# Kernel optimization log

Hardware: AMD Instinct MI355X
Metric: run time of the kernel (lower is better)

Reference implementation:

```python
import jax, jax.numpy as jnp
import numpy as np

MUL0, MUL1, SCALARS_OUT = 16, 16, 128
L0, L1 = MUL0, MUL1 * 3            # 16, 48
PATH_NUMEL = MUL0 * MUL1 * SCALARS_OUT  # 32768 per path, two paths
EPS = 1e-5
# e3nn normalization: irrep_normalization='component' -> alpha = dim(ir_out) = 1;
# path_normalization='element' -> divide by sum over paths to same output of mul1*mul2 = 256+256 = 512.
PATH_COEFF = 1.0 / np.sqrt(512.0)
CG_110 = 1.0 / np.sqrt(3.0)  # wigner_3j(1,1,0)[i,j] = delta_ij/sqrt(3) (unit Frobenius norm)


def layer_norm(x, g, b):
    mu = jnp.mean(x, axis=-1, keepdims=True)
    var = jnp.mean(jnp.square(x - mu), axis=-1, keepdims=True)
    return (x - mu) * jax.lax.rsqrt(var + EPS) * g + b


def ff_block(x, g, b, w1, w2, b2):
    # LayerNorm -> Linear(no bias) -> SiLU -> Linear(bias); residual=False in both uses
    h = jax.nn.silu(layer_norm(x, g, b) @ w1)
    return h @ w2 + b2


def setup_inputs() -> dict:
    key = jax.random.key(0)
    ks = jax.random.split(key, 8)
    N = 2048
    return {
        "x": jax.random.normal(ks[0], (N, L0 + L1), dtype=jnp.float32),
        "we_ln_g": jnp.ones((L0,), jnp.float32),
        "we_ln_b": jnp.zeros((L0,), jnp.float32),
        "we_w1": jax.random.normal(ks[1], (L0, 4 * L0), jnp.float32) / np.sqrt(L0),
        "we_w2": jax.random.normal(ks[2], (4 * L0, 2 * PATH_NUMEL), jnp.float32) / np.sqrt(4 * L0),
        "we_b2": jnp.zeros((2 * PATH_NUMEL,), jnp.float32),
        "om_ln_g": jnp.ones((SCALARS_OUT,), jnp.float32),
        "om_ln_b": jnp.zeros((SCALARS_OUT,), jnp.float32),
        "om_w1": jax.random.normal(ks[3], (SCALARS_OUT, 4 * SCALARS_OUT), jnp.float32) / np.sqrt(SCALARS_OUT),
        "om_w2": jax.random.normal(ks[4], (4 * SCALARS_OUT, 1), jnp.float32) / np.sqrt(4 * SCALARS_OUT),
        "om_b2": jnp.zeros((1,), jnp.float32),
    }


def reference(x, we_ln_g, we_ln_b, we_w1, we_w2, we_b2,
              om_ln_g, om_ln_b, om_w1, om_w2, om_b2):
    N = x.shape[0]
    feats = x[:, :L0]                       # [N, 16] scalars (0e)
    x1 = x[:, L0:].reshape(N, MUL1, 3)      # [N, 16, 3] vectors (1o)

    # per-sample tensor-product weights (shared_weights=False)
    w = ff_block(feats, we_ln_g, we_ln_b, we_w1, we_w2, we_b2)  # [N, 65536]
    w0 = w[:, :PATH_NUMEL].reshape(N, MUL0, MUL0, SCALARS_OUT)
    w1 = w[:, PATH_NUMEL:].reshape(N, MUL1, MUL1, SCALARS_OUT)

    # path 0: 0e x 0e -> 0e  (uvw)
    o0 = jnp.einsum('nu,nv,nuvw->nw', feats, feats, w0)
    # path 1: 1o x 1o -> 0e  (uvw, CG = delta_ij/sqrt(3))
    o1 = jnp.einsum('nui,nvi,nuvw->nw', x1, x1, w1) * CG_110
    tp_out = PATH_COEFF * (o0 + o1)          # [N, 128]

    return ff_block(tp_out, om_ln_g, om_ln_b, om_w1, om_w2, om_b2)  # [N, 1]
```

## Files before the change

### kernel.cpp

```cpp
#include <hip/hip_runtime.h>
#include <hip/hip_bf16.h>
#include <cstdint>

#define EPS 1e-5f
#define PATH_COEFF 0.04419417382415922f
#define CG110     0.5773502691896258f

typedef __bf16 v8bf __attribute__((ext_vector_type(8)));
typedef float  v4f  __attribute__((ext_vector_type(4)));
typedef _Float16 v4h __attribute__((ext_vector_type(4)));
typedef unsigned int v4u __attribute__((ext_vector_type(4)));
typedef unsigned int v2u __attribute__((ext_vector_type(2)));

static __device__ __forceinline__ unsigned short f2bf(float x){
    unsigned int u = __builtin_bit_cast(unsigned int, x);
    u += 0x7fffu + ((u >> 16) & 1u);
    return (unsigned short)(u >> 16);
}
static __device__ __forceinline__ unsigned short f2h(float x){
    return __builtin_bit_cast(unsigned short, (_Float16)x);
}

__global__ __launch_bounds__(256)
void k_pre(const float* __restrict__ w2, const float* __restrict__ b2,
           unsigned short* __restrict__ Vt2,
           const float* __restrict__ om_w1, unsigned short* __restrict__ w1t,
           const float* __restrict__ x, const float* __restrict__ lng,
           const float* __restrict__ lnb, const float* __restrict__ we_w1,
           unsigned short* __restrict__ Q2, float* __restrict__ Ht, int N)
{
    __shared__ __align__(16) unsigned short tile[32][128];
    int b = blockIdx.x;
    int t = threadIdx.x;

    if (b < 260){
        int k    = b >> 2;
        int slab = b & 3;
        const float* srcbase = (k < 64) ? (w2 + (size_t)k * 65536) : b2;
        for (int chunk = 0; chunk < 4; ++chunk){
            int pbase = slab*128 + chunk*32;
            #pragma unroll
            for (int i = 0; i < 4; ++i){
                int g = t + 256*i;
                int ploc = g >> 5, c4 = g & 31;
                const float4 v = *(const float4*)(srcbase + (size_t)(pbase + ploc)*128 + c4*4);
                unsigned int w0 = (unsigned)f2bf(v.x) | ((unsigned)f2bf(v.y) << 16);
                unsigned int w1 = (unsigned)f2bf(v.z) | ((unsigned)f2bf(v.w) << 16);
                *(uint2*)&tile[ploc][c4*4] = make_uint2(w0, w1);
            }
            __syncthreads();
            int w = t & 127, h = t >> 7;
            int ps = slab*4 + chunk;
            unsigned int words[8];
            #pragma unroll
            for (int g2 = 0; g2 < 8; ++g2)
                words[g2] = (unsigned)tile[h*16 + g2*2][w] | ((unsigned)tile[h*16 + g2*2 + 1][w] << 16);
            unsigned short* dq0 = Vt2 + (((size_t)(k*16 + ps)*4 + 2*h    )*128 + w)*8;
            unsigned short* dq1 = Vt2 + (((size_t)(k*16 + ps)*4 + 2*h + 1)*128 + w)*8;
            *(uint4*)dq0 = make_uint4(words[0], words[1], words[2], words[3]);
            *(uint4*)dq1 = make_uint4(words[4], words[5], words[6], words[7]);
            __syncthreads();
        }
    } else if (b < 264){
        int j0 = (b - 260) * 128;
        for (int chunk = 0; chunk < 4; ++chunk){
            #pragma unroll
            for (int i = 0; i < 4; ++i){
                int g = t + 256*i;
                int wloc = g >> 5, c4 = g & 31;
                int w = chunk*32 + wloc;
                const float4 v = *(const float4*)(om_w1 + (size_t)w*512 + j0 + c4*4);
                unsigned int a = (unsigned)f2bf(v.x) | ((unsigned)f2bf(v.y) << 16);
                unsigned int bb = (unsigned)f2bf(v.z) | ((unsigned)f2bf(v.w) << 16);
                *(uint2*)&tile[wloc][c4*4] = make_uint2(a, bb);
            }
            __syncthreads();
            int jl = t & 127, h = t >> 7;
            unsigned int words[8];
            #pragma unroll
            for (int g2 = 0; g2 < 8; ++g2)
                words[g2] = (unsigned)tile[h*16 + g2*2][jl] | ((unsigned)tile[h*16 + g2*2 + 1][jl] << 16);
            unsigned short* dst = w1t + (size_t)(j0 + jl)*128 + chunk*32 + h*16;
            *(uint4*)dst       = make_uint4(words[0], words[1], words[2], words[3]);
            *(uint4*)(dst + 8) = make_uint4(words[4], words[5], words[6], words[7]);
            __syncthreads();
        }
    } else {
        int wv = t >> 6, lane = t & 63;
        int row = (b - 264)*4 + wv;
        const float* xr = x + (size_t)row * 64;
        float f[16]; float mu = 0.f;
        #pragma unroll
        for (int u = 0; u < 16; ++u){ f[u] = xr[u]; mu += f[u]; }
        mu *= (1.f/16.f);
        float var = 0.f;
        #pragma unroll
        for (int u = 0; u < 16; ++u){ float d = f[u] - mu; var += d*d; }
        var *= (1.f/16.f);
        float inv = rsqrtf(var + EPS);
        float lnf[16];
        #pragma unroll
        for (int u = 0; u < 16; ++u) lnf[u] = (f[u]-mu)*inv*lng[u] + lnb[u];
        float h1 = 0.f;
        #pragma unroll
        for (int u = 0; u < 16; ++u) h1 += lnf[u] * we_w1[u*64 + lane];
        float h = h1 / (1.f + expf(-h1));
        Ht[(size_t)lane * N + row] = h;
        if (lane == 0) Ht[(size_t)64 * N + row] = 1.f;

        union { unsigned short qs[8]; uint4 v; } qu;
        #pragma unroll
        for (int j = 0; j < 8; ++j){
            int p = lane*8 + j;
            float q;
            if (p < 256){
                int u = p >> 4, v = p & 15;
                q = PATH_COEFF * f[u] * f[v];
            } else {
                int pp = p - 256;
                int u = pp >> 4, v = pp & 15;
                const float* ya = xr + 16 + u*3;
                const float* yb = xr + 16 + v*3;
                q = (PATH_COEFF * CG110) * (ya[0]*yb[0] + ya[1]*yb[1] + ya[2]*yb[2]);
            }
            qu.qs[j] = f2bf(q);
        }
        int rb = row >> 6, r64 = row & 63;
        int ps = lane >> 2, quad4 = lane & 3;
        *(uint4*)(Q2 + (((size_t)(rb*16 + ps)*4 + quad4)*64 + r64)*8) = qu.v;
    }
}

__global__ __launch_bounds__(128, 4)
void k_main(const unsigned short* __restrict__ Q2, const unsigned short* __restrict__ Vt2,
            const float* __restrict__ Ht, unsigned short* __restrict__ partial, int N)
{
    __shared__ __align__(16) unsigned short Es[2][16*66];
    int kb = blockIdx.x % 65;
    int mb = blockIdx.x / 65;

    int tid  = threadIdx.x;
    int lane = tid & 63, wv = tid >> 6;
    int quad = lane >> 4, l16 = lane & 15;
    int rowbase = mb * 64;
    int wbase = wv * 64;

    const unsigned short* aroot = Q2  + (size_t)mb*32768 + quad*512  + l16*8;
    const unsigned short* broot = Vt2 + (size_t)kb*65536 + quad*1024 + (wbase + l16)*8;

    v4f acc[4][4];
    #pragma unroll
    for (int m=0;m<4;++m)
      #pragma unroll
      for (int n=0;n<4;++n)
        #pragma unroll
        for (int r=0;r<4;++r) acc[m][n][r] = 0.f;

    #pragma unroll 4
    for (int ps = 0; ps < 16; ++ps){
        const unsigned short* ap = aroot + ps*2048;
        const unsigned short* bp = broot + ps*4096;
        v8bf a[4], bb[4];
        #pragma unroll
        for (int m=0;m<4;++m) a[m]  = *(const v8bf*)(ap + m*128);
        #pragma unroll
        for (int n=0;n<4;++n) bb[n] = *(const v8bf*)(bp + n*128);
        #pragma unroll
        for (int m=0;m<4;++m)
          #pragma unroll
          for (int n=0;n<4;++n)
            acc[m][n] = __builtin_amdgcn_mfma_f32_16x16x32_bf16(a[m], bb[n], acc[m][n], 0, 0, 0);
    }

    const float* hp = Ht + (size_t)kb*N + rowbase + quad*4;
    unsigned short* my = Es[wv];
    unsigned short* gp = partial + (size_t)kb*N*128 + (size_t)rowbase*128 + wbase;
    #pragma unroll
    for (int m = 0; m < 4; ++m){
        v4f hv = *(const v4f*)(hp + m*16);
        #pragma unroll
        for (int n = 0; n < 4; ++n)
          #pragma unroll
          for (int r = 0; r < 4; ++r)
            my[(quad*4 + r)*66 + n*16 + l16] = f2h(hv[r]*acc[m][n][r]);
        #pragma unroll
        for (int jj = 0; jj < 2; ++jj){
            int idx = lane*2 + jj;
            int rr = idx >> 3, cc = idx & 7;
            v4u v = *(const v4u*)(Es[wv] + rr*66 + cc*8);
            __builtin_nontemporal_store(v, (v4u*)(gp + (size_t)(m*16 + rr)*128 + cc*8));
        }
    }
}

__global__ __launch_bounds__(128)
void k_red(const unsigned short* __restrict__ partial, const float* __restrict__ g,
           const float* __restrict__ b, unsigned short* __restrict__ lnf, int N)
{
    int t = threadIdx.x;
    int row0 = blockIdx.x * 4;
    int rl = t >> 5, w = (t & 31)*4;
    int row = row0 + rl;

    const unsigned short* p0 = partial + (size_t)row*128 + w;
    float s0=0.f, s1=0.f, s2=0.f, s3=0.f;
    #pragma unroll
    for (int sl = 0; sl < 65; ++sl){
        union { v2u u; v4h h; } cv;
        cv.u = __builtin_nontemporal_load((const v2u*)(p0 + (size_t)sl*N*128));
        s0 += (float)cv.h[0]; s1 += (float)cv.h[1]; s2 += (float)cv.h[2]; s3 += (float)cv.h[3];
    }
    float sum = s0+s1+s2+s3;
    float sq  = s0*s0+s1*s1+s2*s2+s3*s3;
    #pragma unroll
    for (int off=16; off>0; off>>=1){
        sum += __shfl_xor(sum, off, 32);
        sq  += __shfl_xor(sq,  off, 32);
    }
    float mu  = sum * (1.f/128.f);
    float var = sq * (1.f/128.f) - mu*mu;
    float inv = rsqrtf(var + EPS);
    unsigned short o[4];
    o[0] = f2bf((s0-mu)*inv*g[w+0] + b[w+0]);
    o[1] = f2bf((s1-mu)*inv*g[w+1] + b[w+1]);
    o[2] = f2bf((s2-mu)*inv*g[w+2] + b[w+2]);
    o[3] = f2bf((s3-mu)*inv*g[w+3] + b[w+3]);
    *(uint2*)(lnf + (size_t)row*128 + w) = *(uint2*)o;
}

__global__ __launch_bounds__(256)
void k_mlp2(const unsigned short* __restrict__ lnf, const unsigned short* __restrict__ w1t,
            const float* __restrict__ w2, const float* __restrict__ b2,
            float* __restrict__ out, int N)
{
    __shared__ float red2[4][64];
    int tid = threadIdx.x, lane = tid & 63, wv = tid >> 6;
    int quad = lane >> 4, l16 = lane & 15;
    int rowbase = blockIdx.x * 64;
    int jbase = wv * 128;

    v4f acc[4][8];
    #pragma unroll
    for (int m=0;m<4;++m)
      #pragma unroll
      for (int n=0;n<8;++n)
        #pragma unroll
        for (int r=0;r<4;++r) acc[m][n][r] = 0.f;

    #pragma unroll
    for (int ps = 0; ps < 4; ++ps){
        v8bf a[4], bb[8];
        #pragma unroll
        for (int m=0;m<4;++m)
            a[m]  = *(const v8bf*)(lnf + (size_t)(rowbase + m*16 + l16)*128 + ps*32 + quad*8);
        #pragma unroll
        for (int n=0;n<8;++n)
            bb[n] = *(const v8bf*)(w1t + (size_t)(jbase + n*16 + l16)*128 + ps*32 + quad*8);
        #pragma unroll
        for (int m=0;m<4;++m)
          #pragma unroll
          for (int n=0;n<8;++n)
            acc[m][n] = __builtin_amdgcn_mfma_f32_16x16x32_bf16(a[m], bb[n], acc[m][n], 0, 0, 0);
    }

    float w2v[8];
    #pragma unroll
    for (int n=0;n<8;++n) w2v[n] = w2[jbase + n*16 + l16];

    #pragma unroll
    for (int m=0;m<4;++m){
        #pragma unroll
        for (int r=0;r<4;++r){
            float s = 0.f;
            #pragma unroll
            for (int n=0;n<8;++n){
                float v = acc[m][n][r];
                s += (v / (1.f + expf(-v))) * w2v[n];
            }
            #pragma unroll
            for (int off=8; off>0; off>>=1) s += __shfl_xor(s, off, 16);
            if (l16 == 0) red2[wv][m*16 + quad*4 + r] = s;
        }
    }
    __syncthreads();
    if (tid < 64)
        out[rowbase + tid] = red2[0][tid] + red2[1][tid] + red2[2][tid] + red2[3][tid] + b2[0];
}

extern "C" void kernel_launch(void* const* d_in, const int* in_sizes, int n_in,
                              void* d_out, int out_size, void* d_ws, size_t ws_size,
                              hipStream_t stream)
{
    const float* x     = (const float*)d_in[0];
    const float* we_g  = (const float*)d_in[1];
    const float* we_b  = (const float*)d_in[2];
    const float* we_w1 = (const float*)d_in[3];
    const float* we_w2 = (const float*)d_in[4];
    const float* we_b2 = (const float*)d_in[5];
    const float* om_g  = (const float*)d_in[6];
    const float* om_b  = (const float*)d_in[7];
    const float* om_w1 = (const float*)d_in[8];
    const float* om_w2 = (const float*)d_in[9];
    const float* om_b2 = (const float*)d_in[10];

    int N  = in_sizes[0] / 64;

    char* ws = (char*)d_ws;
    size_t offV = 0;
    size_t szV  = (size_t)65*16*4*128*8*2;
    size_t offQ = offV + szV;
    size_t szQ  = (size_t)N*512*2;
    size_t offH = offQ + szQ;
    size_t szH  = (size_t)65*N*4;
    size_t offP = offH + szH;
    size_t szP  = (size_t)65*N*128*2;
    size_t offL = offP + szP;
    size_t szL  = (size_t)N*128*2;
    size_t offW = offL + szL;

    unsigned short* Vt2 = (unsigned short*)(ws + offV);
    unsigned short* Q2  = (unsigned short*)(ws + offQ);
    float* Ht           = (float*)(ws + offH);
    unsigned short* Par = (unsigned short*)(ws + offP);
    unsigned short* Lnf = (unsigned short*)(ws + offL);
    unsigned short* W1t = (unsigned short*)(ws + offW);
    float* out = (float*)d_out;

    hipLaunchKernelGGL(k_pre,  dim3(264 + N/4), dim3(256), 0, stream,
                       we_w2, we_b2, Vt2, om_w1, W1t, x, we_g, we_b, we_w1, Q2, Ht, N);
    hipLaunchKernelGGL(k_main, dim3(32*65),     dim3(128), 0, stream, Q2, Vt2, Ht, Par, N);
    hipLaunchKernelGGL(k_red,  dim3(N/4),       dim3(128), 0, stream, Par, om_g, om_b, Lnf, N);
    hipLaunchKernelGGL(k_mlp2, dim3(N/64),      dim3(256), 0, stream, Lnf, W1t, om_w2, om_b2, out, N);
}
```

Baseline: 151.9 us.

## Double-buffer B tiles through LDS and use 256-thread 2x2 wave blocks in k_main

Each k_main block now runs four waves arranged 2x2 over rows and columns, and the grid is halved to match. Each wave prefetches the next B slab from global memory with contiguous per-lane 16-byte loads into a private double-buffered LDS region, then reads MFMA operands from LDS. The aim is to hide global load latency behind the MFMAs and to make B loads more coalesced. In exchange it adds LDS write and read traffic plus 32KB of LDS per block, which may limit occupancy, and B is still not shared between waves.

```diff
diff --git a/kernel.cpp b/kernel.cpp
--- a/kernel.cpp
+++ b/kernel.cpp
@@ -131,22 +131,24 @@
     }
 }
 
-__global__ __launch_bounds__(128, 4)
+__global__ __launch_bounds__(256, 4)
 void k_main(const unsigned short* __restrict__ Q2, const unsigned short* __restrict__ Vt2,
             const float* __restrict__ Ht, unsigned short* __restrict__ partial, int N)
 {
-    __shared__ __align__(16) unsigned short Es[2][16*66];
+    __shared__ __align__(16) unsigned short Bs[4][2][2048];
     int kb = blockIdx.x % 65;
     int mb = blockIdx.x / 65;
 
     int tid  = threadIdx.x;
     int lane = tid & 63, wv = tid >> 6;
+    int r2 = wv >> 1, c2 = wv & 1;
     int quad = lane >> 4, l16 = lane & 15;
-    int rowbase = mb * 64;
-    int wbase = wv * 64;
-
-    const unsigned short* aroot = Q2  + (size_t)mb*32768 + quad*512  + l16*8;
-    const unsigned short* broot = Vt2 + (size_t)kb*65536 + quad*1024 + (wbase + l16)*8;
+    int rowbase = mb*128 + r2*64;
+    int rb = rowbase >> 6;
+    int wbase = c2*64;
+
+    const unsigned short* aroot = Q2  + (size_t)rb*32768 + quad*512 + l16*8;
+    const unsigned short* broot = Vt2 + (size_t)kb*65536 + wbase*8;
 
     v4f acc[4][4];
     #pragma unroll
@@ -156,24 +158,46 @@
         #pragma unroll
         for (int r=0;r<4;++r) acc[m][n][r] = 0.f;
 
-    #pragma unroll 4
+    unsigned short* bs0 = &Bs[wv][0][0];
+    unsigned short* bs1 = &Bs[wv][1][0];
+
+    {
+        v4u br[4];
+        #pragma unroll
+        for (int r=0;r<4;++r) br[r] = *(const v4u*)(broot + r*1024 + lane*8);
+        #pragma unroll
+        for (int r=0;r<4;++r) *(v4u*)(bs0 + r*512 + lane*8) = br[r];
+    }
+
+    #pragma unroll 2
     for (int ps = 0; ps < 16; ++ps){
+        unsigned short* cur = (ps & 1) ? bs1 : bs0;
+        unsigned short* nxt = (ps & 1) ? bs0 : bs1;
+        v4u nb[4];
+        if (ps < 15){
+            const unsigned short* bp = broot + (ps+1)*4096;
+            #pragma unroll
+            for (int r=0;r<4;++r) nb[r] = *(const v4u*)(bp + r*1024 + lane*8);
+        }
         const unsigned short* ap = aroot + ps*2048;
-        const unsigned short* bp = broot + ps*4096;
         v8bf a[4], bb[4];
         #pragma unroll
-        for (int m=0;m<4;++m) a[m]  = *(const v8bf*)(ap + m*128);
-        #pragma unroll
-        for (int n=0;n<4;++n) bb[n] = *(const v8bf*)(bp + n*128);
+        for (int m=0;m<4;++m) a[m] = *(const v8bf*)(ap + m*128);
+        #pragma unroll
+        for (int n=0;n<4;++n) bb[n] = *(const v8bf*)(cur + quad*512 + (n*16 + l16)*8);
         #pragma unroll
         for (int m=0;m<4;++m)
           #pragma unroll
           for (int n=0;n<4;++n)
             acc[m][n] = __builtin_amdgcn_mfma_f32_16x16x32_bf16(a[m], bb[n], acc[m][n], 0, 0, 0);
+        if (ps < 15){
+            #pragma unroll
+            for (int r=0;r<4;++r) *(v4u*)(nxt + r*512 + lane*8) = nb[r];
+        }
     }
 
     const float* hp = Ht + (size_t)kb*N + rowbase + quad*4;
-    unsigned short* my = Es[wv];
+    unsigned short* Es = &Bs[wv][0][0];
     unsigned short* gp = partial + (size_t)kb*N*128 + (size_t)rowbase*128 + wbase;
     #pragma unroll
     for (int m = 0; m < 4; ++m){
@@ -182,12 +206,12 @@
         for (int n = 0; n < 4; ++n)
           #pragma unroll
           for (int r = 0; r < 4; ++r)
-            my[(quad*4 + r)*66 + n*16 + l16] = f2h(hv[r]*acc[m][n][r]);
+            Es[(quad*4 + r)*66 + n*16 + l16] = f2h(hv[r]*acc[m][n][r]);
         #pragma unroll
         for (int jj = 0; jj < 2; ++jj){
             int idx = lane*2 + jj;
             int rr = idx >> 3, cc = idx & 7;
-            v4u v = *(const v4u*)(Es[wv] + rr*66 + cc*8);
+            v4u v = *(const v4u*)(Es + rr*66 + cc*8);
             __builtin_nontemporal_store(v, (v4u*)(gp + (size_t)(m*16 + rr)*128 + cc*8));
         }
     }
@@ -328,7 +352,7 @@
 
     hipLaunchKernelGGL(k_pre,  dim3(264 + N/4), dim3(256), 0, stream,
                        we_w2, we_b2, Vt2, om_w1, W1t, x, we_g, we_b, we_w1, Q2, Ht, N);
-    hipLaunchKernelGGL(k_main, dim3(32*65),     dim3(128), 0, stream, Q2, Vt2, Ht, Par, N);
+    hipLaunchKernelGGL(k_main, dim3(16*65),     dim3(256), 0, stream, Q2, Vt2, Ht, Par, N);
     hipLaunchKernelGGL(k_red,  dim3(N/4),       dim3(128), 0, stream, Par, om_g, om_b, Lnf, N);
     hipLaunchKernelGGL(k_mlp2, dim3(N/64),      dim3(256), 0, stream, Lnf, W1t, om_w2, om_b2, out, N);
 }
```

Result: no change. 151.5 us (-0.2%).

## Fold per-sample hidden scaling into fp16 A operand and accumulate four k-slabs per block

Applied to the files above, without the earlier changes.

Each main-kernel block now covers four hidden-unit slabs. It scales the Q operand by each sample's SiLU activation before the MFMA and keeps the sum in registers across slabs. This cuts the fp16 partial buffer, and the reduction kernel's reads, from 65 slabs to 17, which removes most of the global memory traffic. Operands move from bf16 to fp16 MFMA so the activation scaling can be applied in half precision, with some risk to numerical range. The weight buffer is padded to 68 slabs, but only 65 are written. The padded slabs rely on zero activations, so uninitialized weights that decode as NaN or Inf could leak into the result.

```diff
diff --git a/kernel.cpp b/kernel.cpp
--- a/kernel.cpp
+++ b/kernel.cpp
@@ -7,10 +7,9 @@
 #define CG110     0.5773502691896258f
 
 typedef __bf16 v8bf __attribute__((ext_vector_type(8)));
+typedef _Float16 v8h __attribute__((ext_vector_type(8)));
 typedef float  v4f  __attribute__((ext_vector_type(4)));
 typedef _Float16 v4h __attribute__((ext_vector_type(4)));
-typedef unsigned int v4u __attribute__((ext_vector_type(4)));
-typedef unsigned int v2u __attribute__((ext_vector_type(2)));
 
 static __device__ __forceinline__ unsigned short f2bf(float x){
     unsigned int u = __builtin_bit_cast(unsigned int, x);
@@ -23,11 +22,11 @@
 
 __global__ __launch_bounds__(256)
 void k_pre(const float* __restrict__ w2, const float* __restrict__ b2,
-           unsigned short* __restrict__ Vt2,
+           unsigned short* __restrict__ Vth,
            const float* __restrict__ om_w1, unsigned short* __restrict__ w1t,
            const float* __restrict__ x, const float* __restrict__ lng,
            const float* __restrict__ lnb, const float* __restrict__ we_w1,
-           unsigned short* __restrict__ Q2, float* __restrict__ Ht, int N)
+           unsigned short* __restrict__ Q2h, unsigned short* __restrict__ Htp, int N)
 {
     __shared__ __align__(16) unsigned short tile[32][128];
     int b = blockIdx.x;
@@ -44,8 +43,8 @@
                 int g = t + 256*i;
                 int ploc = g >> 5, c4 = g & 31;
                 const float4 v = *(const float4*)(srcbase + (size_t)(pbase + ploc)*128 + c4*4);
-                unsigned int w0 = (unsigned)f2bf(v.x) | ((unsigned)f2bf(v.y) << 16);
-                unsigned int w1 = (unsigned)f2bf(v.z) | ((unsigned)f2bf(v.w) << 16);
+                unsigned int w0 = (unsigned)f2h(v.x) | ((unsigned)f2h(v.y) << 16);
+                unsigned int w1 = (unsigned)f2h(v.z) | ((unsigned)f2h(v.w) << 16);
                 *(uint2*)&tile[ploc][c4*4] = make_uint2(w0, w1);
             }
             __syncthreads();
@@ -55,8 +54,8 @@
             #pragma unroll
             for (int g2 = 0; g2 < 8; ++g2)
                 words[g2] = (unsigned)tile[h*16 + g2*2][w] | ((unsigned)tile[h*16 + g2*2 + 1][w] << 16);
-            unsigned short* dq0 = Vt2 + (((size_t)(k*16 + ps)*4 + 2*h    )*128 + w)*8;
-            unsigned short* dq1 = Vt2 + (((size_t)(k*16 + ps)*4 + 2*h + 1)*128 + w)*8;
+            unsigned short* dq0 = Vth + (((size_t)(k*16 + ps)*4 + 2*h    )*128 + w)*8;
+            unsigned short* dq1 = Vth + (((size_t)(k*16 + ps)*4 + 2*h + 1)*128 + w)*8;
             *(uint4*)dq0 = make_uint4(words[0], words[1], words[2], words[3]);
             *(uint4*)dq1 = make_uint4(words[4], words[5], words[6], words[7]);
             __syncthreads();
@@ -105,8 +104,10 @@
         #pragma unroll
         for (int u = 0; u < 16; ++u) h1 += lnf[u] * we_w1[u*64 + lane];
         float h = h1 / (1.f + expf(-h1));
-        Ht[(size_t)lane * N + row] = h;
-        if (lane == 0) Ht[(size_t)64 * N + row] = 1.f;
+        _Float16* hq = (_Float16*)Htp;
+        hq[(size_t)lane * N + row] = (_Float16)h;
+        if (lane == 0) hq[(size_t)64 * N + row] = (_Float16)1.f;
+        if (lane >= 1 && lane <= 3) hq[(size_t)(64 + lane) * N + row] = (_Float16)0.f;
 
         union { unsigned short qs[8]; uint4 v; } qu;
         #pragma unroll
@@ -123,21 +124,22 @@
                 const float* yb = xr + 16 + v*3;
                 q = (PATH_COEFF * CG110) * (ya[0]*yb[0] + ya[1]*yb[1] + ya[2]*yb[2]);
             }
-            qu.qs[j] = f2bf(q);
+            qu.qs[j] = f2h(q);
         }
         int rb = row >> 6, r64 = row & 63;
         int ps = lane >> 2, quad4 = lane & 3;
-        *(uint4*)(Q2 + (((size_t)(rb*16 + ps)*4 + quad4)*64 + r64)*8) = qu.v;
-    }
-}
-
-__global__ __launch_bounds__(128, 4)
-void k_main(const unsigned short* __restrict__ Q2, const unsigned short* __restrict__ Vt2,
-            const float* __restrict__ Ht, unsigned short* __restrict__ partial, int N)
+        *(uint4*)(Q2h + (((size_t)(rb*16 + ps)*4 + quad4)*64 + r64)*8) = qu.v;
+    }
+}
+
+__global__ __launch_bounds__(128, 3)
+void k_main(const unsigned short* __restrict__ Q2h, const unsigned short* __restrict__ Vth,
+            const unsigned short* __restrict__ Htp, unsigned short* __restrict__ partial, int N)
 {
     __shared__ __align__(16) unsigned short Es[2][16*66];
-    int kb = blockIdx.x % 65;
-    int mb = blockIdx.x / 65;
+    int c  = blockIdx.x % 17;
+    int mb = blockIdx.x / 17;
+    int k0 = c*4;
 
     int tid  = threadIdx.x;
     int lane = tid & 63, wv = tid >> 6;
@@ -145,8 +147,16 @@
     int rowbase = mb * 64;
     int wbase = wv * 64;
 
-    const unsigned short* aroot = Q2  + (size_t)mb*32768 + quad*512  + l16*8;
-    const unsigned short* broot = Vt2 + (size_t)kb*65536 + quad*1024 + (wbase + l16)*8;
+    const _Float16* hq = (const _Float16*)Htp;
+    _Float16 hh[4][4];
+    #pragma unroll
+    for (int k = 0; k < 4; ++k)
+      #pragma unroll
+      for (int m = 0; m < 4; ++m)
+        hh[k][m] = hq[(size_t)(k0 + k)*N + rowbase + m*16 + l16];
+
+    const unsigned short* aroot = Q2h + (size_t)mb*32768 + quad*512  + l16*8;
+    const unsigned short* broot = Vth + (size_t)k0*65536 + quad*1024 + (wbase + l16)*8;
 
     v4f acc[4][4];
     #pragma unroll
@@ -156,39 +166,41 @@
         #pragma unroll
         for (int r=0;r<4;++r) acc[m][n][r] = 0.f;
 
-    #pragma unroll 4
     for (int ps = 0; ps < 16; ++ps){
         const unsigned short* ap = aroot + ps*2048;
-        const unsigned short* bp = broot + ps*4096;
-        v8bf a[4], bb[4];
-        #pragma unroll
-        for (int m=0;m<4;++m) a[m]  = *(const v8bf*)(ap + m*128);
-        #pragma unroll
-        for (int n=0;n<4;++n) bb[n] = *(const v8bf*)(bp + n*128);
-        #pragma unroll
-        for (int m=0;m<4;++m)
-          #pragma unroll
-          for (int n=0;n<4;++n)
-            acc[m][n] = __builtin_amdgcn_mfma_f32_16x16x32_bf16(a[m], bb[n], acc[m][n], 0, 0, 0);
-    }
-
-    const float* hp = Ht + (size_t)kb*N + rowbase + quad*4;
-    unsigned short* my = Es[wv];
-    unsigned short* gp = partial + (size_t)kb*N*128 + (size_t)rowbase*128 + wbase;
+        v8h aq[4];
+        #pragma unroll
+        for (int m=0;m<4;++m) aq[m] = *(const v8h*)(ap + m*128);
+        #pragma unroll
+        for (int k = 0; k < 4; ++k){
+            const unsigned short* bp = broot + k*65536 + ps*4096;
+            v8h bb[4];
+            #pragma unroll
+            for (int n=0;n<4;++n) bb[n] = *(const v8h*)(bp + n*128);
+            #pragma unroll
+            for (int m=0;m<4;++m){
+                v8h am = aq[m] * hh[k][m];
+                #pragma unroll
+                for (int n=0;n<4;++n)
+                    acc[m][n] = __builtin_amdgcn_mfma_f32_16x16x32_f16(am, bb[n], acc[m][n], 0, 0, 0);
+            }
+        }
+    }
+
+    unsigned short* Esw = Es[wv];
+    unsigned short* gp = partial + (size_t)c*N*128 + (size_t)rowbase*128 + wbase;
     #pragma unroll
     for (int m = 0; m < 4; ++m){
-        v4f hv = *(const v4f*)(hp + m*16);
         #pragma unroll
         for (int n = 0; n < 4; ++n)
           #pragma unroll
           for (int r = 0; r < 4; ++r)
-            my[(quad*4 + r)*66 + n*16 + l16] = f2h(hv[r]*acc[m][n][r]);
+            Esw[(quad*4 + r)*66 + n*16 + l16] = f2h(acc[m][n][r]);
         #pragma unroll
         for (int jj = 0; jj < 2; ++jj){
             int idx = lane*2 + jj;
             int rr = idx >> 3, cc = idx & 7;
-            v4u v = *(const v4u*)(Es[wv] + rr*66 + cc*8);
-            __builtin_nontemporal_store(v, (v4u*)(gp + (size_t)(m*16 + rr)*128 + cc*8));
+            *(uint4*)(gp + (size_t)(m*16 + rr)*128 + cc*8) = *(const uint4*)(Esw + rr*66 + cc*8);
         }
     }
 }
@@ -205,10 +217,9 @@
     const unsigned short* p0 = partial + (size_t)row*128 + w;
     float s0=0.f, s1=0.f, s2=0.f, s3=0.f;
     #pragma unroll
-    for (int sl = 0; sl < 65; ++sl){
-        union { v2u u; v4h h; } cv;
-        cv.u = __builtin_nontemporal_load((const v2u*)(p0 + (size_t)sl*N*128));
-        s0 += (float)cv.h[0]; s1 += (float)cv.h[1]; s2 += (float)cv.h[2]; s3 += (float)cv.h[3];
+    for (int sl = 0; sl < 17; ++sl){
+        v4h v = *(const v4h*)(p0 + (size_t)sl*N*128);
+        s0 += (float)v[0]; s1 += (float)v[1]; s2 += (float)v[2]; s3 += (float)v[3];
     }
     float sum = s0+s1+s2+s3;
     float sq  = s0*s0+s1*s1+s2*s2+s3*s3;
@@ -307,28 +318,28 @@
 
     char* ws = (char*)d_ws;
     size_t offV = 0;
-    size_t szV  = (size_t)65*16*4*128*8*2;
+    size_t szV  = (size_t)68*65536*2;
     size_t offQ = offV + szV;
     size_t szQ  = (size_t)N*512*2;
     size_t offH = offQ + szQ;
-    size_t szH  = (size_t)65*N*4;
+    size_t szH  = (size_t)68*N*2;
     size_t offP = offH + szH;
-    size_t szP  = (size_t)65*N*128*2;
+    size_t szP  = (size_t)17*N*128*2;
     size_t offL = offP + szP;
     size_t szL  = (size_t)N*128*2;
     size_t offW = offL + szL;
 
-    unsigned short* Vt2 = (unsigned short*)(ws + offV);
-    unsigned short* Q2  = (unsigned short*)(ws + offQ);
-    float* Ht           = (float*)(ws + offH);
+    unsigned short* Vth = (unsigned short*)(ws + offV);
+    unsigned short* Q2h = (unsigned short*)(ws + offQ);
+    unsigned short* Htp = (unsigned short*)(ws + offH);
     unsigned short* Par = (unsigned short*)(ws + offP);
     unsigned short* Lnf = (unsigned short*)(ws + offL);
     unsigned short* W1t = (unsigned short*)(ws + offW);
     float* out = (float*)d_out;
 
     hipLaunchKernelGGL(k_pre,  dim3(264 + N/4), dim3(256), 0, stream,
-                       we_w2, we_b2, Vt2, om_w1, W1t, x, we_g, we_b, we_w1, Q2, Ht, N);
-    hipLaunchKernelGGL(k_main, dim3(32*65),     dim3(128), 0, stream, Q2, Vt2, Ht, Par, N);
+                       we_w2, we_b2, Vth, om_w1, W1t, x, we_g, we_b, we_w1, Q2h, Htp, N);
+    hipLaunchKernelGGL(k_main, dim3(32*17),     dim3(128), 0, stream, Q2h, Vth, Htp, Par, N);
     hipLaunchKernelGGL(k_red,  dim3(N/4),       dim3(128), 0, stream, Par, om_g, om_b, Lnf, N);
     hipLaunchKernelGGL(k_mlp2, dim3(N/64),      dim3(256), 0, stream, Lnf, W1t, om_w2, om_b2, out, N);
 }
```

Result: slower. 158.1 us (+4.1%).
